# Kernel optimization log

Hardware: AMD Instinct MI355X
Metric: run time of the kernel (lower is better)

Reference implementation:

```python
import jax, jax.numpy as jnp
import numpy as np

D_IN, D, H, NL, DFF = 128, 256, 4, 4, 1024
N, B, L = 32768, 64, 672


def setup_inputs() -> dict:
    key = jax.random.key(0)
    ks = jax.random.split(key, 12)
    s = 0.02
    return {
        "dom_embeddings": jax.random.normal(ks[0], (N, D_IN), jnp.float32),
        "dom_to_event_idx": jax.random.randint(ks[1], (N,), 0, B, jnp.int32),
        "batch_size": B,
        "seq_len": L,
        "proj_w": jax.random.normal(ks[2], (D_IN, D), jnp.float32) * s,
        "proj_b": jnp.zeros((D,), jnp.float32),
        "cls_token": jax.random.normal(ks[3], (D,), jnp.float32),
        "ln1_g": jnp.ones((NL, D), jnp.float32),
        "ln1_b": jnp.zeros((NL, D), jnp.float32),
        "qkv_w": jax.random.normal(ks[4], (NL, D, 3 * D), jnp.float32) * s,
        "qkv_b": jnp.zeros((NL, 3 * D), jnp.float32),
        "out_w": jax.random.normal(ks[5], (NL, D, D), jnp.float32) * s,
        "out_b": jnp.zeros((NL, D), jnp.float32),
        "ln2_g": jnp.ones((NL, D), jnp.float32),
        "ln2_b": jnp.zeros((NL, D), jnp.float32),
        "ff1_w": jax.random.normal(ks[6], (NL, D, DFF), jnp.float32) * s,
        "ff1_b": jnp.zeros((NL, DFF), jnp.float32),
        "ff2_w": jax.random.normal(ks[7], (NL, DFF, D), jnp.float32) * s,
        "ff2_b": jnp.zeros((NL, D), jnp.float32),
        "head1_w": jax.random.normal(ks[8], (D, D), jnp.float32) * s,
        "head1_b": jnp.zeros((D,), jnp.float32),
        "head2_w": jax.random.normal(ks[9], (D, 3), jnp.float32) * s,
        "head2_b": jnp.zeros((3,), jnp.float32),
    }


def _ln(x, g, b):
    m = jnp.mean(x, axis=-1, keepdims=True)
    v = jnp.var(x, axis=-1, keepdims=True)
    return (x - m) / jnp.sqrt(v + 1e-5) * g + b


def _forward(dom_embeddings, proj_w, proj_b, cls_token, ln1_g, ln1_b, qkv_w, qkv_b,
             out_w, out_b, ln2_g, ln2_b, ff1_w, ff1_b, ff2_w, ff2_b,
             head1_w, head1_b, head2_w, head2_b, idx, batch_size, seq_len):
    n = idx.shape[0]
    d = proj_w.shape[1]
    dh = d // H
    x = dom_embeddings @ proj_w + proj_b  # (N, d)

    # per-segment rank (replaces the python for-loop): stable argsort + cumsum of counts
    counts = jnp.zeros((batch_size,), jnp.int32).at[idx].add(1)
    starts = jnp.cumsum(counts) - counts
    order = jnp.argsort(idx)  # jax sort is stable -> preserves in-event order
    rank_sorted = jnp.arange(n, dtype=jnp.int32) - starts[idx[order]]
    positions = jnp.zeros((n,), jnp.int32).at[order].set(rank_sorted)

    # scatter into padded batch; slot 0 is cls (note: cls KEY stays masked, as in torch code)
    bt = jnp.zeros((batch_size, seq_len, d), x.dtype).at[:, 0, :].set(cls_token)
    bt = bt.at[idx, positions + 1].set(x)
    pad = jnp.ones((batch_size, seq_len), bool).at[idx, positions + 1].set(False)
    bias = jnp.where(pad, -jnp.inf, 0.0).astype(x.dtype)[:, None, None, :]  # (B,1,1,L)

    h = bt
    for i in range(NL):  # norm_first pre-LN encoder layers
        y = _ln(h, ln1_g[i], ln1_b[i])
        qkv = y @ qkv_w[i] + qkv_b[i]
        q, k, v = jnp.split(qkv, 3, axis=-1)
        q = q.reshape(batch_size, seq_len, H, dh)
        k = k.reshape(batch_size, seq_len, H, dh)
        v = v.reshape(batch_size, seq_len, H, dh)
        scores = jnp.einsum('bqhd,bkhd->bhqk', q, k) * (1.0 / np.sqrt(dh))
        attn = jax.nn.softmax(scores + bias, axis=-1)
        o = jnp.einsum('bhqk,bkhd->bqhd', attn, v).reshape(batch_size, seq_len, d)
        h = h + o @ out_w[i] + out_b[i]
        z = _ln(h, ln2_g[i], ln2_b[i])
        h = h + jax.nn.relu(z @ ff1_w[i] + ff1_b[i]) @ ff2_w[i] + ff2_b[i]

    cls = h[:, 0, :]
    p = jax.nn.relu(cls @ head1_w + head1_b) @ head2_w + head2_b
    return p / jnp.sqrt(jnp.sum(p * p, axis=1, keepdims=True))


def reference(dom_embeddings, dom_to_event_idx, batch_size, seq_len, proj_w, proj_b,
              cls_token, ln1_g, ln1_b, qkv_w, qkv_b, out_w, out_b, ln2_g, ln2_b,
              ff1_w, ff1_b, ff2_w, ff2_b, head1_w, head1_b, head2_w, head2_b):
    return _forward(dom_embeddings, proj_w, proj_b, cls_token, ln1_g, ln1_b, qkv_w,
                    qkv_b, out_w, out_b, ln2_g, ln2_b, ff1_w, ff1_b, ff2_w, ff2_b,
                    head1_w, head1_b, head2_w, head2_b,
                    dom_to_event_idx, batch_size, seq_len)
```

## Files before the change

### kernel.cpp

```cpp
#include <hip/hip_runtime.h>
#include <cstdint>
#include <cstddef>

#define NDOM   32768
#define DIN    128
#define DMODEL 256
#define NHEAD  4
#define NLAYER 4
#define DFFN   1024
#define BATCH  64
#define SEQ    672
#define DHEAD  64
#define MC     33024
#define MTILES 258

typedef unsigned short u16;
typedef __attribute__((ext_vector_type(8))) short bf8;
typedef __attribute__((ext_vector_type(4))) float f4;

__device__ inline u16 f2b(float x) {
    union { float f; unsigned u; } c; c.f = x;
    unsigned r = c.u + 0x7fffu + ((c.u >> 16) & 1u);
    return (u16)(r >> 16);
}

__device__ inline void gload16(const void* g, const void* l) {
    __builtin_amdgcn_global_load_lds(
        (const __attribute__((address_space(1))) void*)g,
        (__attribute__((address_space(3))) void*)l, 16, 0, 0);
}


__global__ void k_zero_counts(int* __restrict__ counts) {
    if (threadIdx.x < BATCH) counts[threadIdx.x] = 0;
}

__global__ void k_pos(const int* __restrict__ idx, int* __restrict__ counts,
                      int* __restrict__ pos) {
    int i = blockIdx.x * blockDim.x + threadIdx.x;
    if (i < NDOM) pos[i] = atomicAdd(&counts[idx[i]], 1);
}

__global__ void k_base(const int* __restrict__ counts, int* __restrict__ base) {
    const int lane = threadIdx.x;
    const int c = counts[lane];
    int s = c;
    #pragma unroll
    for (int off = 1; off < 64; off <<= 1) {
        int t = __shfl_up(s, off);
        if (lane >= off) s += t;
    }
    base[lane] = lane + (s - c);
    if (lane == 63) base[64] = 64 + s;
}

__global__ void k_rmap(const int* __restrict__ idx, const int* __restrict__ pos,
                       const int* __restrict__ base, int* __restrict__ rmap) {
    int i = blockIdx.x * 256 + threadIdx.x;
    if (i < NDOM) {
        int p = pos[i] + 1;
        rmap[i] = (p < SEQ) ? base[idx[i]] + p : (MC - 1);
    }
}

__global__ void k_init_cls(const int* __restrict__ base, const float* __restrict__ cls,
                           float* __restrict__ h) {
    h[(size_t)base[blockIdx.x] * DMODEL + threadIdx.x] = cls[threadIdx.x];
}

__global__ void k_b16(const float* __restrict__ x, u16* __restrict__ y, int n4) {
    int i = blockIdx.x * 256 + threadIdx.x;
    if (i < n4) {
        float4 v = ((const float4*)x)[i];
        ushort4 o;
        o.x = f2b(v.x); o.y = f2b(v.y); o.z = f2b(v.z); o.w = f2b(v.w);
        ((ushort4*)y)[i] = o;
    }
}

__global__ __launch_bounds__(256) void k_wt_all(
    const float* __restrict__ projw, const float* __restrict__ qkvw,
    const float* __restrict__ outw,  const float* __restrict__ ff1w,
    const float* __restrict__ ff2w,
    u16* __restrict__ wpj, u16* __restrict__ wq, u16* __restrict__ wo,
    u16* __restrict__ w1,  u16* __restrict__ w2)
{
    __shared__ float t[64][65];
    const int tile = blockIdx.x;
    const float* W; u16* D; int K, N, local;
    if (tile < 8)        { W = projw; D = wpj; K = 128;  N = 256;  local = tile; }
    else if (tile < 200) { int l = (tile-8)/48;   local = (tile-8)%48;
                           W = qkvw + (size_t)l*196608; D = wq + (size_t)l*196608; K = 256;  N = 768; }
    else if (tile < 264) { int l = (tile-200)/16; local = (tile-200)%16;
                           W = outw + (size_t)l*65536;  D = wo + (size_t)l*65536;  K = 256;  N = 256; }
    else if (tile < 520) { int l = (tile-264)/64; local = (tile-264)%64;
                           W = ff1w + (size_t)l*262144; D = w1 + (size_t)l*262144; K = 256;  N = 1024; }
    else                 { int l = (tile-520)/64; local = (tile-520)%64;
                           W = ff2w + (size_t)l*262144; D = w2 + (size_t)l*262144; K = 1024; N = 256; }
    const int ntn = N >> 6;
    const int tk = local / ntn, tn = local % ntn;
    const int r = threadIdx.x >> 6, c = threadIdx.x & 63;
    #pragma unroll 4
    for (int rr = r; rr < 64; rr += 4)
        t[rr][c] = W[(size_t)(tk*64 + rr) * N + tn*64 + c];
    __syncthreads();
    #pragma unroll 4
    for (int rr = r; rr < 64; rr += 4)
        D[(size_t)(tn*64 + rr) * K + tk*64 + c] = f2b(t[c][rr]);
}


__global__ __launch_bounds__(256) void k_ln_bf(
    const float* __restrict__ x, const float* __restrict__ g,
    const float* __restrict__ bt, u16* __restrict__ y)
{
    const int row  = blockIdx.x * 4 + (threadIdx.x >> 6);
    const int lane = threadIdx.x & 63;
    float4 v = ((const float4*)(x + (size_t)row * DMODEL))[lane];
    float s = v.x + v.y + v.z + v.w;
    #pragma unroll
    for (int off = 32; off >= 1; off >>= 1) s += __shfl_xor(s, off);
    const float m = s * (1.f / DMODEL);
    const float d0 = v.x - m, d1 = v.y - m, d2 = v.z - m, d3 = v.w - m;
    float q = d0*d0 + d1*d1 + d2*d2 + d3*d3;
    #pragma unroll
    for (int off = 32; off >= 1; off >>= 1) q += __shfl_xor(q, off);
    const float rstd = rsqrtf(q * (1.f / DMODEL) + 1e-5f);
    const float4 gv = ((const float4*)g)[lane];
    const float4 bv = ((const float4*)bt)[lane];
    ushort4 o;
    o.x = f2b(d0 * rstd * gv.x + bv.x);
    o.y = f2b(d1 * rstd * gv.y + bv.y);
    o.z = f2b(d2 * rstd * gv.z + bv.z);
    o.w = f2b(d3 * rstd * gv.w + bv.w);
    ((ushort4*)(y + (size_t)row * DMODEL))[lane] = o;
}


template<int RELU, int OBF, int OF32, int SCAT>
__global__ __launch_bounds__(256) void k_gemm_bf(
    const u16* __restrict__ A, const u16* __restrict__ Bt,
    const float* __restrict__ bias, float* __restrict__ Cf,
    u16* __restrict__ Cb, const int* __restrict__ rmap, int K, int N)
{
    __shared__ u16 As[8192];
    __shared__ u16 Bs[8192];
    const int tid = threadIdx.x;
    const int w = tid >> 6, lane = tid & 63;
    const int lr = lane & 15, lg = lane >> 4;
    const int m0 = blockIdx.y * 128, n0 = blockIdx.x * 128;
    const int wm = (w >> 1) * 64, wn = (w & 1) * 64;

    const f4 zf = {0.f, 0.f, 0.f, 0.f};
    f4 acc[4][4];
    #pragma unroll
    for (int i = 0; i < 4; ++i)
        #pragma unroll
        for (int j = 0; j < 4; ++j) acc[i][j] = zf;

    const int srow8 = lane >> 3;
    const int sq = lane & 7;

    for (int k0 = 0; k0 < K; k0 += 64) {
        #pragma unroll
        for (int c = 0; c < 4; ++c) {
            const int chunk = w * 4 + c;
            const int row = chunk * 8 + srow8;
            const int ks = k0 + ((sq ^ (row & 7)) << 3);
            gload16(A  + (size_t)(m0 + row) * K + ks, (const char*)As + chunk * 1024);
            gload16(Bt + (size_t)(n0 + row) * K + ks, (const char*)Bs + chunk * 1024);
        }
        __syncthreads();
        #pragma unroll
        for (int kk = 0; kk < 2; ++kk) {
            bf8 af[4], bg[4];
            #pragma unroll
            for (int f = 0; f < 4; ++f) {
                const int ra = wm + f * 16 + lr;
                af[f] = *(const bf8*)((const char*)As + ra * 128 +
                        ((((kk << 2) | lg) ^ (ra & 7)) << 4));
                const int rb = wn + f * 16 + lr;
                bg[f] = *(const bf8*)((const char*)Bs + rb * 128 +
                        ((((kk << 2) | lg) ^ (rb & 7)) << 4));
            }
            #pragma unroll
            for (int fm = 0; fm < 4; ++fm)
                #pragma unroll
                for (int fn = 0; fn < 4; ++fn)
                    acc[fm][fn] = __builtin_amdgcn_mfma_f32_16x16x32_bf16(
                        af[fm], bg[fn], acc[fm][fn], 0, 0, 0);
        }
        __syncthreads();
    }

    float bv[4];
    #pragma unroll
    for (int fn = 0; fn < 4; ++fn) bv[fn] = bias[n0 + wn + fn * 16 + lr];
    #pragma unroll
    for (int fm = 0; fm < 4; ++fm)
        #pragma unroll
        for (int j = 0; j < 4; ++j) {
            const int row = m0 + wm + fm * 16 + lg * 4 + j;
            const int orow = SCAT ? rmap[row] : row;
            #pragma unroll
            for (int fn = 0; fn < 4; ++fn) {
                float v = acc[fm][fn][j] + bv[fn];
                if (RELU) v = fmaxf(v, 0.f);
                const size_t off = (size_t)orow * N + n0 + wn + fn * 16 + lr;
                if (OF32)  Cf[off] = v;
                if (OBF)   Cb[off] = f2b(v);
            }
        }
}


template<int LNF>
__global__ __launch_bounds__(512) void k_gemm_ln(
    const u16* __restrict__ A, const u16* __restrict__ Bt,
    const float* __restrict__ bias, float* __restrict__ h,
    u16* __restrict__ ybf, const float* __restrict__ lng,
    const float* __restrict__ lnb, int K)
{
    __shared__ u16 As[8192];
    __shared__ u16 Bs[16384];
    __shared__ float red[8][136];
    const int tid = threadIdx.x;
    const int w = tid >> 6, lane = tid & 63;
    const int lr = lane & 15, lg = lane >> 4;
    const int m0 = blockIdx.x * 128;
    const int wm = (w >> 2) * 64, wn = (w & 3) * 64;

    const f4 zf = {0.f, 0.f, 0.f, 0.f};
    f4 acc[4][4];
    #pragma unroll
    for (int i = 0; i < 4; ++i)
        #pragma unroll
        for (int j = 0; j < 4; ++j) acc[i][j] = zf;

    const int srow8 = lane >> 3;
    const int sq = lane & 7;

    for (int k0 = 0; k0 < K; k0 += 64) {
        #pragma unroll
        for (int c = 0; c < 2; ++c) {
            const int chunk = w * 2 + c;
            const int row = chunk * 8 + srow8;
            const int ks = k0 + ((sq ^ (row & 7)) << 3);
            gload16(A + (size_t)(m0 + row) * K + ks, (const char*)As + chunk * 1024);
        }
        #pragma unroll
        for (int c = 0; c < 4; ++c) {
            const int chunk = w * 4 + c;
            const int row = chunk * 8 + srow8;
            const int ks = k0 + ((sq ^ (row & 7)) << 3);
            gload16(Bt + (size_t)row * K + ks, (const char*)Bs + chunk * 1024);
        }
        __syncthreads();
        #pragma unroll
        for (int kk = 0; kk < 2; ++kk) {
            bf8 af[4], bg[4];
            #pragma unroll
            for (int f = 0; f < 4; ++f) {
                const int ra = wm + f * 16 + lr;
                af[f] = *(const bf8*)((const char*)As + ra * 128 +
                        ((((kk << 2) | lg) ^ (ra & 7)) << 4));
                const int rb = wn + f * 16 + lr;
                bg[f] = *(const bf8*)((const char*)Bs + rb * 128 +
                        ((((kk << 2) | lg) ^ (rb & 7)) << 4));
            }
            #pragma unroll
            for (int fm = 0; fm < 4; ++fm)
                #pragma unroll
                for (int fn = 0; fn < 4; ++fn)
                    acc[fm][fn] = __builtin_amdgcn_mfma_f32_16x16x32_bf16(
                        af[fm], bg[fn], acc[fm][fn], 0, 0, 0);
        }
        __syncthreads();
    }

    float bv[4];
    #pragma unroll
    for (int fn = 0; fn < 4; ++fn) bv[fn] = bias[wn + fn * 16 + lr];
    float sr[4][4], s2r[4][4];
    #pragma unroll
    for (int fm = 0; fm < 4; ++fm)
        #pragma unroll
        for (int j = 0; j < 4; ++j) {
            const int row = m0 + wm + fm * 16 + lg * 4 + j;
            float s = 0.f, s2 = 0.f;
            #pragma unroll
            for (int fn = 0; fn < 4; ++fn) {
                float v = acc[fm][fn][j] + bv[fn];
                v += h[(size_t)row * DMODEL + wn + fn * 16 + lr];
                acc[fm][fn][j] = v;
                s += v; s2 += v * v;
            }
            if (LNF) {
                #pragma unroll
                for (int off = 1; off <= 8; off <<= 1) {
                    s  += __shfl_xor(s, off);
                    s2 += __shfl_xor(s2, off);
                }
            }
            sr[fm][j] = s; s2r[fm][j] = s2;
        }

    if (LNF) {
        if (lr == 0) {
            #pragma unroll
            for (int fm = 0; fm < 4; ++fm)
                #pragma unroll
                for (int j = 0; j < 4; ++j) {
                    const int rL = wm + fm * 16 + lg * 4 + j;
                    red[(w & 3) * 2 + 0][rL] = sr[fm][j];
                    red[(w & 3) * 2 + 1][rL] = s2r[fm][j];
                }
        }
        __syncthreads();
        float gl[4], bl[4];
        #pragma unroll
        for (int fn = 0; fn < 4; ++fn) {
            gl[fn] = lng[wn + fn * 16 + lr];
            bl[fn] = lnb[wn + fn * 16 + lr];
        }
        #pragma unroll
        for (int fm = 0; fm < 4; ++fm)
            #pragma unroll
            for (int j = 0; j < 4; ++j) {
                const int rL = wm + fm * 16 + lg * 4 + j;
                const int row = m0 + rL;
                const float S  = red[0][rL] + red[2][rL] + red[4][rL] + red[6][rL];
                const float S2 = red[1][rL] + red[3][rL] + red[5][rL] + red[7][rL];
                const float mean = S * (1.f / DMODEL);
                const float var  = S2 * (1.f / DMODEL) - mean * mean;
                const float rstd = rsqrtf(var + 1e-5f);
                #pragma unroll
                for (int fn = 0; fn < 4; ++fn) {
                    const float v = acc[fm][fn][j];
                    const size_t off = (size_t)row * DMODEL + wn + fn * 16 + lr;
                    h[off] = v;
                    ybf[off] = f2b((v - mean) * rstd * gl[fn] + bl[fn]);
                }
            }
    } else {
        #pragma unroll
        for (int fm = 0; fm < 4; ++fm)
            #pragma unroll
            for (int j = 0; j < 4; ++j) {
                const int row = m0 + wm + fm * 16 + lg * 4 + j;
                #pragma unroll
                for (int fn = 0; fn < 4; ++fn)
                    h[(size_t)row * DMODEL + wn + fn * 16 + lr] = acc[fm][fn][j];
            }
    }
}


__global__ __launch_bounds__(512) void k_attn_mfma(
    const u16* __restrict__ qkv, const int* __restrict__ counts,
    const int* __restrict__ base, u16* __restrict__ out)
{
    __shared__ u16 Ks[4096];
    __shared__ u16 Vt[4096];
    __shared__ u16 Ps[8][1024];
    const int tid = threadIdx.x;
    const int w = tid >> 6, lane = tid & 63;
    const int lr = lane & 15, lg = lane >> 4;
    const int L = blockIdx.x;
    const int b = (L & 7) * 8 + (L >> 3) / 24;
    const int r = (L >> 3) % 24;
    const int qt = r >> 2, hh = r & 3;
    const int q0 = qt * 128;
    const int kmax = min(counts[b], SEQ - 1);
    if (q0 > kmax) return;
    const int ntiles = (kmax + 64) >> 6;
    const size_t bb = (size_t)base[b];

    const int qrow = q0 + w * 16 + lr;
    const size_t qoff = (bb + qrow) * 768 + hh * 64 + (lg << 3);
    const bf8 qf0 = *(const bf8*)(qkv + qoff);
    const bf8 qf1 = *(const bf8*)(qkv + qoff + 32);

    const f4 zf = {0.f, 0.f, 0.f, 0.f};
    f4 o_[4];
    #pragma unroll
    for (int fn = 0; fn < 4; ++fn) o_[fn] = zf;
    float mrow = -INFINITY, ssum = 0.f;

    for (int kt = 0; kt < ntiles; ++kt) {
        const int k0 = kt * 64;
        {
            const int row = w * 8 + (lane >> 3);
            const int q = lane & 7;
            gload16(qkv + (bb + k0 + row) * 768 + 256 + hh * 64 + ((q ^ (row & 7)) << 3),
                    (const char*)Ks + w * 1024);
        }
        {
            const int kk2 = (tid & 31) * 2;
            const int dh0 = (tid >> 5) * 4;
            const ushort4 v0 = *(const ushort4*)(qkv + (bb + k0 + kk2) * 768 + 512 + hh * 64 + dh0);
            const ushort4 v1 = *(const ushort4*)(qkv + (bb + k0 + kk2 + 1) * 768 + 512 + hh * 64 + dh0);
            const u16* pv0 = (const u16*)&v0;
            const u16* pv1 = (const u16*)&v1;
            #pragma unroll
            for (int e = 0; e < 4; ++e) {
                const int d = dh0 + e;
                const unsigned pk = (unsigned)pv0[e] | ((unsigned)pv1[e] << 16);
                *(unsigned*)((char*)Vt + d * 128 +
                    ((((kk2 >> 3) ^ (d & 7)) << 4)) + ((kk2 & 7) << 1)) = pk;
            }
        }
        __syncthreads();

        f4 sf[4];
        #pragma unroll
        for (int fk = 0; fk < 4; ++fk) sf[fk] = zf;
        #pragma unroll
        for (int kk = 0; kk < 2; ++kk) {
            const bf8 qf = kk ? qf1 : qf0;
            #pragma unroll
            for (int fk = 0; fk < 4; ++fk) {
                const int rk = fk * 16 + lr;
                const bf8 kf = *(const bf8*)((const char*)Ks + rk * 128 +
                        ((((kk << 2) | lg) ^ (rk & 7)) << 4));
                sf[fk] = __builtin_amdgcn_mfma_f32_16x16x32_bf16(kf, qf, sf[fk], 0, 0, 0);
            }
        }

        float sv[4][4];
        float pmax = -INFINITY;
        if (k0 >= 1 && k0 + 63 <= kmax) {
            #pragma unroll
            for (int fk = 0; fk < 4; ++fk)
                #pragma unroll
                for (int j = 0; j < 4; ++j) {
                    const float x = sf[fk][j] * 0.125f;
                    sv[fk][j] = x;
                    pmax = fmaxf(pmax, x);
                }
        } else {
            #pragma unroll
            for (int fk = 0; fk < 4; ++fk)
                #pragma unroll
                for (int j = 0; j < 4; ++j) {
                    const int key = k0 + fk * 16 + lg * 4 + j;
                    const float x = (key >= 1 && key <= kmax) ? sf[fk][j] * 0.125f : -INFINITY;
                    sv[fk][j] = x;
                    pmax = fmaxf(pmax, x);
                }
        }
        pmax = fmaxf(pmax, __shfl_xor(pmax, 16));
        pmax = fmaxf(pmax, __shfl_xor(pmax, 32));

        if (!__all(pmax <= mrow + 8.f)) {
            const float mnew = fmaxf(mrow, pmax);
            const float fac = __expf(mrow - mnew);
            mrow = mnew;
            ssum *= fac;
            #pragma unroll
            for (int j = 0; j < 4; ++j) {
                const float fj = __shfl(fac, lg * 4 + j);
                #pragma unroll
                for (int fn = 0; fn < 4; ++fn) o_[fn][j] *= fj;
            }
        }

        float tsum = 0.f;
        #pragma unroll
        for (int fk = 0; fk < 4; ++fk) {
            const float p0 = __expf(sv[fk][0] - mrow);
            const float p1 = __expf(sv[fk][1] - mrow);
            const float p2 = __expf(sv[fk][2] - mrow);
            const float p3 = __expf(sv[fk][3] - mrow);
            tsum += p0 + p1 + p2 + p3;
            ushort4 pk;
            pk.x = f2b(p0); pk.y = f2b(p1); pk.z = f2b(p2); pk.w = f2b(p3);
            *(ushort4*)((char*)Ps[w] + lr * 128 +
                (((((fk << 1) | (lg >> 1)) ^ (lr & 7)) << 4)) + ((lg & 1) << 3)) = pk;
        }
        tsum += __shfl_xor(tsum, 16);
        tsum += __shfl_xor(tsum, 32);
        ssum += tsum;
        __syncthreads();

        #pragma unroll
        for (int kk = 0; kk < 2; ++kk) {
            const bf8 pa = *(const bf8*)((const char*)Ps[w] + lr * 128 +
                    ((((kk << 2) | lg) ^ (lr & 7)) << 4));
            #pragma unroll
            for (int fn = 0; fn < 4; ++fn) {
                const int rv = fn * 16 + lr;
                const bf8 vf = *(const bf8*)((const char*)Vt + rv * 128 +
                        ((((kk << 2) | lg) ^ (rv & 7)) << 4));
                o_[fn] = __builtin_amdgcn_mfma_f32_16x16x32_bf16(pa, vf, o_[fn], 0, 0, 0);
            }
        }
        __syncthreads();
    }

    const float inv = 1.f / ssum;
    #pragma unroll
    for (int j = 0; j < 4; ++j) {
        const float ij = __shfl(inv, lg * 4 + j);
        const int qr = q0 + w * 16 + lg * 4 + j;
        if (qr <= kmax) {
            #pragma unroll
            for (int fn = 0; fn < 4; ++fn)
                out[(bb + qr) * DMODEL + hh * 64 + fn * 16 + lr] = f2b(o_[fn][j] * ij);
        }
    }
}


__global__ __launch_bounds__(256) void k_head(
    const float* __restrict__ h, const int* __restrict__ base,
    const float* __restrict__ w1, const float* __restrict__ b1,
    const float* __restrict__ w2, const float* __restrict__ b2,
    float* __restrict__ out)
{
    __shared__ float cbuf[DMODEL];
    __shared__ float p1[DMODEL];
    __shared__ float p2[3];
    const int b = blockIdx.x, tid = threadIdx.x;
    cbuf[tid] = h[(size_t)base[b] * DMODEL + tid];
    __syncthreads();
    float acc = b1[tid];
    #pragma unroll 8
    for (int k = 0; k < DMODEL; ++k) acc = fmaf(cbuf[k], w1[k * DMODEL + tid], acc);
    p1[tid] = fmaxf(acc, 0.f);
    __syncthreads();
    if (tid < 3) {
        float a = b2[tid];
        for (int k = 0; k < DMODEL; ++k) a = fmaf(p1[k], w2[k * 3 + tid], a);
        p2[tid] = a;
    }
    __syncthreads();
    if (tid < 3) {
        float n2 = p2[0]*p2[0] + p2[1]*p2[1] + p2[2]*p2[2];
        out[b * 3 + tid] = p2[tid] * rsqrtf(n2);
    }
}


extern "C" void kernel_launch(void* const* d_in, const int* in_sizes, int n_in,
                              void* d_out, int out_size, void* d_ws, size_t ws_size,
                              hipStream_t stream) {
    const float* emb   = (const float*)d_in[0];
    const int*   idx   = (const int*)d_in[1];
    const float* projw = (const float*)d_in[4];
    const float* projb = (const float*)d_in[5];
    const float* cls   = (const float*)d_in[6];
    const float* ln1g  = (const float*)d_in[7];
    const float* ln1b  = (const float*)d_in[8];
    const float* qkvw  = (const float*)d_in[9];
    const float* qkvb  = (const float*)d_in[10];
    const float* outw  = (const float*)d_in[11];
    const float* outb  = (const float*)d_in[12];
    const float* ln2g  = (const float*)d_in[13];
    const float* ln2b  = (const float*)d_in[14];
    const float* ff1w  = (const float*)d_in[15];
    const float* ff1b  = (const float*)d_in[16];
    const float* ff2w  = (const float*)d_in[17];
    const float* ff2b  = (const float*)d_in[18];
    const float* h1w   = (const float*)d_in[19];
    const float* h1b   = (const float*)d_in[20];
    const float* h2w   = (const float*)d_in[21];
    const float* h2b   = (const float*)d_in[22];
    float* out = (float*)d_out;

    char* ws = (char*)d_ws;
    int*   counts = (int*)ws;
    int*   base   = (int*)(ws + 256);
    int*   pos    = (int*)(ws + 1024);
    int*   rmap   = (int*)(ws + 132096);
    float* h      = (float*)(ws + 263168);
    u16*   ybf    = (u16*)(ws + 34079744);
    u16*   qkvc   = (u16*)(ws + 50988032);
    u16*   ffb    = (u16*)(ws + 101712896);
    u16*   wq     = (u16*)(ws + 169346048);
    u16*   wo     = (u16*)(ws + 170918912);
    u16*   w1     = (u16*)(ws + 171443200);
    u16*   w2     = (u16*)(ws + 173540352);
    u16*   wpj    = (u16*)(ws + 175637504);
    u16*   embbf  = qkvc;

    k_zero_counts<<<1, 64, 0, stream>>>(counts);
    k_pos<<<NDOM / 256, 256, 0, stream>>>(idx, counts, pos);
    k_base<<<1, 64, 0, stream>>>(counts, base);
    k_rmap<<<NDOM / 256, 256, 0, stream>>>(idx, pos, base, rmap);
    k_b16<<<(NDOM * DIN / 4) / 256, 256, 0, stream>>>(emb, embbf, NDOM * DIN / 4);
    k_wt_all<<<776, 256, 0, stream>>>(projw, qkvw, outw, ff1w, ff2w,
                                      wpj, wq, wo, w1, w2);
    k_init_cls<<<BATCH, 256, 0, stream>>>(base, cls, h);
    k_gemm_bf<0,0,1,1><<<dim3(2, 256), 256, 0, stream>>>(
        embbf, wpj, projb, h, nullptr, rmap, DIN, DMODEL);
    k_ln_bf<<<MC / 4, 256, 0, stream>>>(h, ln1g, ln1b, ybf);

    for (int l = 0; l < NLAYER; ++l) {
        k_gemm_bf<0,1,0,0><<<dim3(6, MTILES), 256, 0, stream>>>(
            ybf, wq + (size_t)l * 196608, qkvb + l * 768, nullptr, qkvc, nullptr, 256, 768);
        k_attn_mfma<<<1536, 512, 0, stream>>>(qkvc, counts, base, ybf);
        k_gemm_ln<1><<<MTILES, 512, 0, stream>>>(
            ybf, wo + (size_t)l * 65536, outb + l * DMODEL, h, ybf,
            ln2g + l * DMODEL, ln2b + l * DMODEL, 256);
        k_gemm_bf<1,1,0,0><<<dim3(8, MTILES), 256, 0, stream>>>(
            ybf, w1 + (size_t)l * 262144, ff1b + l * DFFN, nullptr, ffb, nullptr, 256, 1024);
        if (l < NLAYER - 1)
            k_gemm_ln<1><<<MTILES, 512, 0, stream>>>(
                ffb, w2 + (size_t)l * 262144, ff2b + l * DMODEL, h, ybf,
                ln1g + (l + 1) * DMODEL, ln1b + (l + 1) * DMODEL, 1024);
        else
            k_gemm_ln<0><<<MTILES, 512, 0, stream>>>(
                ffb, w2 + (size_t)l * 262144, ff2b + l * DMODEL, h, nullptr,
                nullptr, nullptr, 1024);
    }

    k_head<<<BATCH, 256, 0, stream>>>(h, base, h1w, h1b, h2w, h2b, out);
}
```

Measured before the change: 1.086 ms.

## Restructure GEMM+LayerNorm kernel: 64-row tiles, full-row waves, double-buffered LDS

The fused GEMM+residual+LayerNorm kernel now uses 64-row tiles with 256 threads. Each wave owns 16 full rows across all 256 output columns, so the LayerNorm reduction needs only intra-wave shuffles and no shared-memory reduction pass or extra barrier. Global-to-LDS loads are double-buffered so the next K tile loads while the current one computes, and the grid doubles to 516 blocks for better CU coverage. In exchange each wave reloads the whole B tile from LDS per k-step with one A fragment, so LDS read traffic per MFMA rises, and 16 accumulators plus bias/gamma/beta arrays raise register pressure.

Result: no change. 1.077 ms (-0.8%).

```diff
diff --git a/kernel.cpp b/kernel.cpp
--- a/kernel.cpp
+++ b/kernel.cpp
@@ -215,143 +215,118 @@
 
 
 template<int LNF>
-__global__ __launch_bounds__(512) void k_gemm_ln(
+__global__ __launch_bounds__(256) void k_gemm_ln(
     const u16* __restrict__ A, const u16* __restrict__ Bt,
     const float* __restrict__ bias, float* __restrict__ h,
     u16* __restrict__ ybf, const float* __restrict__ lng,
     const float* __restrict__ lnb, int K)
 {
-    __shared__ u16 As[8192];
-    __shared__ u16 Bs[16384];
-    __shared__ float red[8][136];
+    __shared__ u16 AS[2][4096];
+    __shared__ u16 BS[2][16384];
     const int tid = threadIdx.x;
     const int w = tid >> 6, lane = tid & 63;
     const int lr = lane & 15, lg = lane >> 4;
-    const int m0 = blockIdx.x * 128;
-    const int wm = (w >> 2) * 64, wn = (w & 3) * 64;
+    const int m0 = blockIdx.x * 64;
+    const int srow8 = lane >> 3, sq = lane & 7;
 
     const f4 zf = {0.f, 0.f, 0.f, 0.f};
-    f4 acc[4][4];
-    #pragma unroll
-    for (int i = 0; i < 4; ++i)
-        #pragma unroll
-        for (int j = 0; j < 4; ++j) acc[i][j] = zf;
-
-    const int srow8 = lane >> 3;
-    const int sq = lane & 7;
-
-    for (int k0 = 0; k0 < K; k0 += 64) {
+    f4 acc[16];
+    #pragma unroll
+    for (int fn = 0; fn < 16; ++fn) acc[fn] = zf;
+
+    const int NT = K >> 6;
+
+    {
         #pragma unroll
         for (int c = 0; c < 2; ++c) {
             const int chunk = w * 2 + c;
             const int row = chunk * 8 + srow8;
-            const int ks = k0 + ((sq ^ (row & 7)) << 3);
-            gload16(A + (size_t)(m0 + row) * K + ks, (const char*)As + chunk * 1024);
-        }
-        #pragma unroll
-        for (int c = 0; c < 4; ++c) {
-            const int chunk = w * 4 + c;
+            const int ks = (sq ^ (row & 7)) << 3;
+            gload16(A + (size_t)(m0 + row) * K + ks, (const char*)AS[0] + chunk * 1024);
+        }
+        #pragma unroll
+        for (int c = 0; c < 8; ++c) {
+            const int chunk = w * 8 + c;
             const int row = chunk * 8 + srow8;
-            const int ks = k0 + ((sq ^ (row & 7)) << 3);
-            gload16(Bt + (size_t)row * K + ks, (const char*)Bs + chunk * 1024);
+            const int ks = (sq ^ (row & 7)) << 3;
+            gload16(Bt + (size_t)row * K + ks, (const char*)BS[0] + chunk * 1024);
+        }
+    }
+    __syncthreads();
+
+    int cur = 0;
+    for (int t = 0; t < NT; ++t) {
+        if (t + 1 < NT) {
+            const int k0 = (t + 1) << 6;
+            #pragma unroll
+            for (int c = 0; c < 2; ++c) {
+                const int chunk = w * 2 + c;
+                const int row = chunk * 8 + srow8;
+                const int ks = k0 + ((sq ^ (row & 7)) << 3);
+                gload16(A + (size_t)(m0 + row) * K + ks, (const char*)AS[cur ^ 1] + chunk * 1024);
+            }
+            #pragma unroll
+            for (int c = 0; c < 8; ++c) {
+                const int chunk = w * 8 + c;
+                const int row = chunk * 8 + srow8;
+                const int ks = k0 + ((sq ^ (row & 7)) << 3);
+                gload16(Bt + (size_t)row * K + ks, (const char*)BS[cur ^ 1] + chunk * 1024);
+            }
+        }
+        #pragma unroll
+        for (int kk = 0; kk < 2; ++kk) {
+            const int ra = w * 16 + lr;
+            const bf8 af = *(const bf8*)((const char*)AS[cur] + ra * 128 +
+                    ((((kk << 2) | lg) ^ (ra & 7)) << 4));
+            #pragma unroll
+            for (int fn = 0; fn < 16; ++fn) {
+                const int rb = fn * 16 + lr;
+                const bf8 bg = *(const bf8*)((const char*)BS[cur] + rb * 128 +
+                        ((((kk << 2) | lg) ^ (rb & 7)) << 4));
+                acc[fn] = __builtin_amdgcn_mfma_f32_16x16x32_bf16(af, bg, acc[fn], 0, 0, 0);
+            }
         }
         __syncthreads();
-        #pragma unroll
-        for (int kk = 0; kk < 2; ++kk) {
-            bf8 af[4], bg[4];
-            #pragma unroll
-            for (int f = 0; f < 4; ++f) {
-                const int ra = wm + f * 16 + lr;
-                af[f] = *(const bf8*)((const char*)As + ra * 128 +
-                        ((((kk << 2) | lg) ^ (ra & 7)) << 4));
-                const int rb = wn + f * 16 + lr;
-                bg[f] = *(const bf8*)((const char*)Bs + rb * 128 +
-                        ((((kk << 2) | lg) ^ (rb & 7)) << 4));
-            }
-            #pragma unroll
-            for (int fm = 0; fm < 4; ++fm)
-                #pragma unroll
-                for (int fn = 0; fn < 4; ++fn)
-                    acc[fm][fn] = __builtin_amdgcn_mfma_f32_16x16x32_bf16(
-                        af[fm], bg[fn], acc[fm][fn], 0, 0, 0);
-        }
-        __syncthreads();
-    }
-
-    float bv[4];
-    #pragma unroll
-    for (int fn = 0; fn < 4; ++fn) bv[fn] = bias[wn + fn * 16 + lr];
-    float sr[4][4], s2r[4][4];
-    #pragma unroll
-    for (int fm = 0; fm < 4; ++fm)
-        #pragma unroll
-        for (int j = 0; j < 4; ++j) {
-            const int row = m0 + wm + fm * 16 + lg * 4 + j;
-            float s = 0.f, s2 = 0.f;
-            #pragma unroll
-            for (int fn = 0; fn < 4; ++fn) {
-                float v = acc[fm][fn][j] + bv[fn];
-                v += h[(size_t)row * DMODEL + wn + fn * 16 + lr];
-                acc[fm][fn][j] = v;
-                s += v; s2 += v * v;
-            }
-            if (LNF) {
-                #pragma unroll
-                for (int off = 1; off <= 8; off <<= 1) {
-                    s  += __shfl_xor(s, off);
-                    s2 += __shfl_xor(s2, off);
-                }
-            }
-            sr[fm][j] = s; s2r[fm][j] = s2;
-        }
-
-    if (LNF) {
-        if (lr == 0) {
-            #pragma unroll
-            for (int fm = 0; fm < 4; ++fm)
-                #pragma unroll
-                for (int j = 0; j < 4; ++j) {
-                    const int rL = wm + fm * 16 + lg * 4 + j;
-                    red[(w & 3) * 2 + 0][rL] = sr[fm][j];
-                    red[(w & 3) * 2 + 1][rL] = s2r[fm][j];
-                }
-        }
-        __syncthreads();
-        float gl[4], bl[4];
-        #pragma unroll
-        for (int fn = 0; fn < 4; ++fn) {
-            gl[fn] = lng[wn + fn * 16 + lr];
-            bl[fn] = lnb[wn + fn * 16 + lr];
-        }
-        #pragma unroll
-        for (int fm = 0; fm < 4; ++fm)
-            #pragma unroll
-            for (int j = 0; j < 4; ++j) {
-                const int rL = wm + fm * 16 + lg * 4 + j;
-                const int row = m0 + rL;
-                const float S  = red[0][rL] + red[2][rL] + red[4][rL] + red[6][rL];
-                const float S2 = red[1][rL] + red[3][rL] + red[5][rL] + red[7][rL];
-                const float mean = S * (1.f / DMODEL);
-                const float var  = S2 * (1.f / DMODEL) - mean * mean;
-                const float rstd = rsqrtf(var + 1e-5f);
-                #pragma unroll
-                for (int fn = 0; fn < 4; ++fn) {
-                    const float v = acc[fm][fn][j];
-                    const size_t off = (size_t)row * DMODEL + wn + fn * 16 + lr;
-                    h[off] = v;
-                    ybf[off] = f2b((v - mean) * rstd * gl[fn] + bl[fn]);
-                }
-            }
-    } else {
-        #pragma unroll
-        for (int fm = 0; fm < 4; ++fm)
-            #pragma unroll
-            for (int j = 0; j < 4; ++j) {
-                const int row = m0 + wm + fm * 16 + lg * 4 + j;
-                #pragma unroll
-                for (int fn = 0; fn < 4; ++fn)
-                    h[(size_t)row * DMODEL + wn + fn * 16 + lr] = acc[fm][fn][j];
-            }
+        cur ^= 1;
+    }
+
+    float bv[16], gl[16], bl[16];
+    #pragma unroll
+    for (int fn = 0; fn < 16; ++fn) {
+        bv[fn] = bias[fn * 16 + lr];
+        if (LNF) { gl[fn] = lng[fn * 16 + lr]; bl[fn] = lnb[fn * 16 + lr]; }
+    }
+    #pragma unroll
+    for (int j = 0; j < 4; ++j) {
+        const int row = m0 + w * 16 + lg * 4 + j;
+        float s = 0.f, s2 = 0.f;
+        #pragma unroll
+        for (int fn = 0; fn < 16; ++fn) {
+            float v = acc[fn][j] + bv[fn] + h[(size_t)row * DMODEL + fn * 16 + lr];
+            acc[fn][j] = v;
+            s += v; s2 += v * v;
+        }
+        if (LNF) {
+            #pragma unroll
+            for (int off = 1; off <= 8; off <<= 1) {
+                s  += __shfl_xor(s, off);
+                s2 += __shfl_xor(s2, off);
+            }
+            const float mean = s * (1.f / DMODEL);
+            const float var  = s2 * (1.f / DMODEL) - mean * mean;
+            const float rstd = rsqrtf(var + 1e-5f);
+            #pragma unroll
+            for (int fn = 0; fn < 16; ++fn) {
+                const size_t off2 = (size_t)row * DMODEL + fn * 16 + lr;
+                const float v = acc[fn][j];
+                h[off2] = v;
+                ybf[off2] = f2b((v - mean) * rstd * gl[fn] + bl[fn]);
+            }
+        } else {
+            #pragma unroll
+            for (int fn = 0; fn < 16; ++fn)
+                h[(size_t)row * DMODEL + fn * 16 + lr] = acc[fn][j];
+        }
     }
 }
 
@@ -600,17 +575,17 @@
         k_gemm_bf<0,1,0,0><<<dim3(6, MTILES), 256, 0, stream>>>(
             ybf, wq + (size_t)l * 196608, qkvb + l * 768, nullptr, qkvc, nullptr, 256, 768);
         k_attn_mfma<<<1536, 512, 0, stream>>>(qkvc, counts, base, ybf);
-        k_gemm_ln<1><<<MTILES, 512, 0, stream>>>(
+        k_gemm_ln<1><<<MC / 64, 256, 0, stream>>>(
             ybf, wo + (size_t)l * 65536, outb + l * DMODEL, h, ybf,
             ln2g + l * DMODEL, ln2b + l * DMODEL, 256);
         k_gemm_bf<1,1,0,0><<<dim3(8, MTILES), 256, 0, stream>>>(
             ybf, w1 + (size_t)l * 262144, ff1b + l * DFFN, nullptr, ffb, nullptr, 256, 1024);
         if (l < NLAYER - 1)
-            k_gemm_ln<1><<<MTILES, 512, 0, stream>>>(
+            k_gemm_ln<1><<<MC / 64, 256, 0, stream>>>(
                 ffb, w2 + (size_t)l * 262144, ff2b + l * DMODEL, h, ybf,
                 ln1g + (l + 1) * DMODEL, ln1b + (l + 1) * DMODEL, 1024);
         else
-            k_gemm_ln<0><<<MTILES, 512, 0, stream>>>(
+            k_gemm_ln<0><<<MC / 64, 256, 0, stream>>>(
                 ffb, w2 + (size_t)l * 262144, ff2b + l * DMODEL, h, nullptr,
                 nullptr, nullptr, 1024);
     }
```
